# Kernel tuning notes

Hardware: AMD Instinct MI355X
Metric: run time of the kernel (lower is better)

## Reference

```python
import jax, jax.numpy as jnp
import numpy as np

D_MODEL = 1024
NUM_HEADS = 16
DEPTH = D_MODEL // NUM_HEADS


def setup_inputs() -> dict:
    key = jax.random.key(0)
    ks = jax.random.split(key, 11)
    B, S, D = 2, 2048, D_MODEL
    s = 1.0 / np.sqrt(D)
    inp = {
        'x': jax.random.normal(ks[0], (B, S, D), jnp.float32),
        'pH': jax.random.normal(ks[1], (B, 1, 1), jnp.float32),
        'Wq': jax.random.normal(ks[2], (D, D), jnp.float32) * s,
        'bq': jnp.zeros((D,), jnp.float32),
        'Wk': jax.random.normal(ks[3], (D, D), jnp.float32) * s,
        'bk': jnp.zeros((D,), jnp.float32),
        'Wv': jax.random.normal(ks[4], (D, D), jnp.float32) * s,
        'bv': jnp.zeros((D,), jnp.float32),
        'Wo': jax.random.normal(ks[5], (D, D), jnp.float32) * s,
        'bo': jnp.zeros((D,), jnp.float32),
    }
    return inp


def reference(x, pH, Wq, bq, Wk, bk, Wv, bv, Wo, bo):
    B, S, D = x.shape
    H, dh = NUM_HEADS, DEPTH
    # QKV projections -> [B, H, S, dh]
    def proj(W, b):
        return (x @ W + b).reshape(B, S, H, dh).transpose(0, 2, 1, 3)
    q = proj(Wq, bq)
    k = proj(Wk, bk)
    v = proj(Wv, bv)
    # scores [B, H, S, S] with additive per-sample pH bias broadcast over heads/positions
    scores = jnp.einsum('bhqd,bhkd->bhqk', q, k) / jnp.sqrt(jnp.asarray(dh, x.dtype))
    scores = scores + pH[:, :, :, None]  # [B,1,1,1] broadcasts to [B,H,S,S]
    attn = jax.nn.softmax(scores, axis=-1)
    out = jnp.einsum('bhqk,bhkd->bhqd', attn, v)  # [B,H,S,dh]
    out = out.transpose(0, 2, 1, 3).reshape(B, S, D)
    return out @ Wo + bo  # dropout p=0.0 -> identity
```

## Files before the change

### kernel.cpp

```cpp
#include <hip/hip_runtime.h>
#include <hip/hip_bf16.h>
#include <math.h>

#define BATCH 2
#define SEQ   2048
#define DMODEL 1024
#define NHEADS 16
#define DHEAD 64
#define MROWS (BATCH*SEQ)

typedef __attribute__((ext_vector_type(8))) short bf16x8;
typedef __attribute__((ext_vector_type(4))) short bf16x4;
typedef __attribute__((ext_vector_type(4))) float f32x4;

__device__ __forceinline__ short f2bf(float f) {
    union { float f; unsigned u; } c; c.f = f;
    unsigned r = (c.u + 0x7fffu + ((c.u >> 16) & 1u)) >> 16;
    return (short)r;
}
__device__ __forceinline__ float bf2f(short h) {
    union { unsigned u; float f; } c; c.u = ((unsigned)(unsigned short)h) << 16;
    return c.f;
}

__device__ __forceinline__ void async_ld16(const void* g, void* l) {
    __builtin_amdgcn_global_load_lds(
        (const __attribute__((address_space(1))) unsigned*)g,
        (__attribute__((address_space(3))) unsigned*)l, 16, 0, 0);
}

__global__ __launch_bounds__(256) void prep(
    const float* __restrict__ x, short* __restrict__ xhi,
    const float* __restrict__ W0, const float* __restrict__ W1,
    const float* __restrict__ W2, const float* __restrict__ W3,
    short* __restrict__ oqkv, short* __restrict__ oo)
{
    __shared__ float T[64][65];
    const int tid = threadIdx.x;
    if (blockIdx.x < 2048) {
        const int i = blockIdx.x * 256 + tid;
        const float4* p = (const float4*)x + (size_t)i * 2;
        float4 a = p[0], b = p[1];
        float v[8] = {a.x, a.y, a.z, a.w, b.x, b.y, b.z, b.w};
        bf16x8 H;
        #pragma unroll
        for (int j = 0; j < 8; ++j) H[j] = f2bf(v[j]);
        *((bf16x8*)xhi + i) = H;
        return;
    }
    const int bi = blockIdx.x - 2048;
    const int z = bi >> 8;
    const int t = bi & 255;
    const float* W = (z == 0) ? W0 : (z == 1) ? W1 : (z == 2) ? W2 : W3;
    short* out = (z < 3) ? (oqkv + (size_t)z * 1024 * 1024) : oo;
    const int n0 = (t & 15) * 64, k0 = (t >> 4) * 64;
    #pragma unroll
    for (int i = 0; i < 16; ++i) {
        const int idx = tid + i * 256;
        const int r = idx >> 6, c = idx & 63;
        T[r][c] = W[(size_t)(k0 + r) * DMODEL + n0 + c];
    }
    __syncthreads();
    #pragma unroll
    for (int i = 0; i < 4; ++i) {
        const int idx = tid + i * 256;
        const int r = idx >> 4, g = idx & 15;
        bf16x4 H;
        #pragma unroll
        for (int j = 0; j < 4; ++j)
            H[j] = f2bf(T[g * 4 + j][r]);
        *(bf16x4*)(out + (size_t)(n0 + r) * DMODEL + k0 + g * 4) = H;
    }
}

#define GBK 64

__global__ __launch_bounds__(256) void mfma_gemm(
    const short* __restrict__ Ahi, const short* __restrict__ Bthi,
    const float* __restrict__ b0, const float* __restrict__ b1, const float* __restrict__ b2,
    short* __restrict__ oqh, short* __restrict__ okh, short* __restrict__ ovh,
    float* __restrict__ outf, int mode, float qscale)
{
    __shared__ short Ah[128 * GBK], Bh[128 * GBK];

    const int tid  = threadIdx.x;
    const int lane = tid & 63;
    const int w    = tid >> 6;
    const int quad = lane >> 4;
    const int l15  = lane & 15;
    const int wr   = w >> 1, wc = w & 1;
    const int m0   = blockIdx.y * 128;
    const int n0   = blockIdx.x * 128;
    const int K    = DMODEL;

    f32x4 acc[4][4] = {};

    int srow[4], spos[4];
    #pragma unroll
    for (int j = 0; j < 4; ++j) {
        const int c = w * 256 + j * 64 + lane;
        srow[j] = c >> 3;
        spos[j] = (c & 7) ^ (srow[j] & 7);
    }

    for (int k0 = 0; k0 < K; k0 += GBK) {
        __syncthreads();
        #pragma unroll
        for (int j = 0; j < 4; ++j) {
            const int cB = (w * 256 + j * 64) * 8;
            async_ld16(Ahi + (size_t)(m0 + srow[j]) * K + k0 + spos[j] * 8, Ah + cB);
            async_ld16(Bthi + (size_t)(n0 + srow[j]) * K + k0 + spos[j] * 8, Bh + cB);
        }
        __syncthreads();

        #pragma unroll
        for (int s = 0; s < 2; ++s) {
            bf16x8 afh[4], bfh[4];
            #pragma unroll
            for (int mi = 0; mi < 4; ++mi) {
                const int row = wr * 64 + mi * 16 + l15;
                const int pos = (s * 4 + quad) ^ (row & 7);
                afh[mi] = *(const bf16x8*)(Ah + row * GBK + pos * 8);
            }
            #pragma unroll
            for (int ni = 0; ni < 4; ++ni) {
                const int row = wc * 64 + ni * 16 + l15;
                const int pos = (s * 4 + quad) ^ (row & 7);
                bfh[ni] = *(const bf16x8*)(Bh + row * GBK + pos * 8);
            }
            #pragma unroll
            for (int mi = 0; mi < 4; ++mi)
                #pragma unroll
                for (int ni = 0; ni < 4; ++ni)
                    acc[mi][ni] = __builtin_amdgcn_mfma_f32_16x16x32_bf16(
                        afh[mi], bfh[ni], acc[mi][ni], 0, 0, 0);
        }
    }

    const int nbase = n0 + wc * 64;
    if (mode == 1) {
        #pragma unroll
        for (int mi = 0; mi < 4; ++mi)
            #pragma unroll
            for (int ni = 0; ni < 4; ++ni)
                #pragma unroll
                for (int r = 0; r < 4; ++r) {
                    const int m = m0 + wr * 64 + mi * 16 + quad * 4 + r;
                    const int nn = nbase + ni * 16 + l15;
                    outf[(size_t)m * DMODEL + nn] = acc[mi][ni][r] + b0[nn];
                }
    } else {
        __syncthreads();
        short* scr = (w < 2) ? (Ah + w * 4096) : (Bh + (w - 2) * 4096);
        const int which = nbase >> 10;
        const int hh = (nbase & 1023) >> 6;
        const int mb = m0 + wr * 64;
        const int b = mb >> 11, sbase = mb & (SEQ - 1);

        if (which < 2) {
            const float* bias = which ? b1 : b0;
            short* dstp = which ? okh : oqh;
            const float scl = which ? 1.0f : qscale;
            #pragma unroll
            for (int mi = 0; mi < 4; ++mi)
                #pragma unroll
                for (int ni = 0; ni < 4; ++ni)
                    #pragma unroll
                    for (int r = 0; r < 4; ++r) {
                        const int sloc = mi * 16 + quad * 4 + r;
                        const int dloc = ni * 16 + l15;
                        const int nn = (nbase + ni * 16 + l15) & 1023;
                        scr[sloc * 64 + (((dloc >> 3) ^ (sloc & 7)) * 8) + (dloc & 7)] =
                            f2bf((acc[mi][ni][r] + bias[nn]) * scl);
                    }
            #pragma unroll
            for (int i = 0; i < 8; ++i) {
                const int sloc = i * 8 + (lane >> 3);
                const int cph = (lane & 7) ^ (sloc & 7);
                bf16x8 row = *(const bf16x8*)(scr + sloc * 64 + cph * 8);
                const int dloc = (lane & 7) * 8;
                *(bf16x8*)(dstp + ((size_t)(b * NHEADS + hh) * SEQ + sbase + sloc) * DHEAD + dloc) = row;
            }
        } else {
            #pragma unroll
            for (int mi = 0; mi < 4; ++mi)
                #pragma unroll
                for (int ni = 0; ni < 4; ++ni)
                    #pragma unroll
                    for (int r = 0; r < 4; ++r) {
                        const int sloc = mi * 16 + quad * 4 + r;
                        const int dloc = ni * 16 + l15;
                        const int nn = (nbase + ni * 16 + l15) & 1023;
                        scr[dloc * 64 + (((sloc >> 3) ^ (dloc & 7)) * 8) + (sloc & 7)] =
                            f2bf(acc[mi][ni][r] + b2[nn]);
                    }
            #pragma unroll
            for (int i = 0; i < 8; ++i) {
                const int dloc = i * 8 + (lane >> 3);
                const int cph = (lane & 7) ^ (dloc & 7);
                bf16x8 row = *(const bf16x8*)(scr + dloc * 64 + cph * 8);
                const int sg = sbase + (lane & 7) * 8;
                *(bf16x8*)(ovh + ((size_t)(b * NHEADS + hh) * DHEAD + dloc) * SEQ + sg) = row;
            }
        }
    }
}

__global__ __launch_bounds__(256) void attn_mfma(
    const short* __restrict__ Qh_g, const short* __restrict__ Kh_g,
    const short* __restrict__ Vth_g,
    short* __restrict__ op0, short* __restrict__ op1,
    float* __restrict__ l0g, float* __restrict__ l1g)
{
    __shared__ short Ksh[4096];
    __shared__ short Vsh[4096];
    __shared__ short Ph[4][2][1024];

    const int tid  = threadIdx.x;
    const int lane = tid & 63;
    const int w    = tid >> 6;
    const int quad = lane >> 4;
    const int l15  = lane & 15;

    const int bh    = blockIdx.x & 31;
    const int sk    = (blockIdx.x >> 5) & 1;
    const int qtile = blockIdx.x >> 6;
    const int q0    = qtile * 128 + w * 32;
    const size_t kvb = (size_t)bh * SEQ * DHEAD;

    bf16x8 ones;
    #pragma unroll
    for (int j = 0; j < 8; ++j) ones[j] = (short)0x3f80;

    bf16x8 qA[2], qB[2];
    {
        const size_t qrA = kvb + (size_t)(q0 + l15) * DHEAD;
        const size_t qrB = kvb + (size_t)(q0 + 16 + l15) * DHEAD;
        qA[0] = *(const bf16x8*)(Qh_g + qrA + quad * 8);
        qA[1] = *(const bf16x8*)(Qh_g + qrA + 32 + quad * 8);
        qB[0] = *(const bf16x8*)(Qh_g + qrB + quad * 8);
        qB[1] = *(const bf16x8*)(Qh_g + qrB + 32 + quad * 8);
    }

    const bool isv = (w >= 2);
    short* dst = isv ? Vsh : Ksh;
    int srow[4], spos[4];
    #pragma unroll
    for (int j = 0; j < 4; ++j) {
        const int c = (w & 1) * 256 + j * 64 + lane;
        srow[j] = c >> 3;
        spos[j] = (c & 7) ^ (srow[j] & 7);
    }

    f32x4 oA[4] = {}, oB[4] = {};
    f32x4 lAv = {}, lBv = {};

    const int kb0 = sk * (SEQ / 2), kb1 = kb0 + SEQ / 2;
    for (int kb = kb0; kb < kb1; kb += 64) {
        __syncthreads();
        {
            const short* src = isv ? (Vth_g + kvb + kb) : (Kh_g + kvb + (size_t)kb * DHEAD);
            #pragma unroll
            for (int j = 0; j < 4; ++j) {
                const short* g = src + (isv ? ((size_t)srow[j] * SEQ + spos[j] * 8)
                                            : ((size_t)srow[j] * DHEAD + spos[j] * 8));
                async_ld16(g, dst + ((w & 1) * 256 + j * 64) * 8);
            }
        }
        __syncthreads();

        #pragma unroll
        for (int mf = 0; mf < 4; ++mf) {
            const int row = mf * 16 + l15;
            const int sw = row & 7;
            bf16x8 kh0 = *(const bf16x8*)(Ksh + row * 64 + ((quad ^ sw) * 8));
            bf16x8 kh1 = *(const bf16x8*)(Ksh + row * 64 + (((4 + quad) ^ sw) * 8));
            f32x4 cA = {}, cB = {};
            cA = __builtin_amdgcn_mfma_f32_16x16x32_bf16(kh0, qA[0], cA, 0, 0, 0);
            cA = __builtin_amdgcn_mfma_f32_16x16x32_bf16(kh1, qA[1], cA, 0, 0, 0);
            cB = __builtin_amdgcn_mfma_f32_16x16x32_bf16(kh0, qB[0], cB, 0, 0, 0);
            cB = __builtin_amdgcn_mfma_f32_16x16x32_bf16(kh1, qB[1], cB, 0, 0, 0);

            unsigned uA[4], uB[4];
            #pragma unroll
            for (int r = 0; r < 4; ++r) {
                union { float f; unsigned u; } p;
                p.f = __builtin_amdgcn_exp2f(cA[r]);
                uA[r] = p.u;
                p.f = __builtin_amdgcn_exp2f(cB[r]);
                uB[r] = p.u;
            }
            uint2 pkA, pkB;
            pkA.x = __builtin_amdgcn_perm(uA[1], uA[0], 0x07060302u);
            pkA.y = __builtin_amdgcn_perm(uA[3], uA[2], 0x07060302u);
            pkB.x = __builtin_amdgcn_perm(uB[1], uB[0], 0x07060302u);
            pkB.y = __builtin_amdgcn_perm(uB[3], uB[2], 0x07060302u);
            const int pc = (mf * 2 + (quad >> 1)) ^ (l15 & 7);
            const int paddr = l15 * 64 + pc * 8 + (quad & 1) * 4;
            *(uint2*)(&Ph[w][0][paddr]) = pkA;
            *(uint2*)(&Ph[w][1][paddr]) = pkB;
        }

        const int psw = l15 & 7;
        bf16x8 pA0 = *(const bf16x8*)(&Ph[w][0][l15 * 64 + ((quad ^ psw) * 8)]);
        bf16x8 pA1 = *(const bf16x8*)(&Ph[w][0][l15 * 64 + (((4 + quad) ^ psw) * 8)]);
        bf16x8 pB0 = *(const bf16x8*)(&Ph[w][1][l15 * 64 + ((quad ^ psw) * 8)]);
        bf16x8 pB1 = *(const bf16x8*)(&Ph[w][1][l15 * 64 + (((4 + quad) ^ psw) * 8)]);

        lAv = __builtin_amdgcn_mfma_f32_16x16x32_bf16(pA0, ones, lAv, 0, 0, 0);
        lAv = __builtin_amdgcn_mfma_f32_16x16x32_bf16(pA1, ones, lAv, 0, 0, 0);
        lBv = __builtin_amdgcn_mfma_f32_16x16x32_bf16(pB0, ones, lBv, 0, 0, 0);
        lBv = __builtin_amdgcn_mfma_f32_16x16x32_bf16(pB1, ones, lBv, 0, 0, 0);

        #pragma unroll
        for (int nf = 0; nf < 4; ++nf) {
            const int row = nf * 16 + l15;
            const int sw = row & 7;
            bf16x8 vh0 = *(const bf16x8*)(Vsh + row * 64 + ((quad ^ sw) * 8));
            bf16x8 vh1 = *(const bf16x8*)(Vsh + row * 64 + (((4 + quad) ^ sw) * 8));
            f32x4 cA = oA[nf], cB = oB[nf];
            cA = __builtin_amdgcn_mfma_f32_16x16x32_bf16(pA0, vh0, cA, 0, 0, 0);
            cA = __builtin_amdgcn_mfma_f32_16x16x32_bf16(pA1, vh1, cA, 0, 0, 0);
            cB = __builtin_amdgcn_mfma_f32_16x16x32_bf16(pB0, vh0, cB, 0, 0, 0);
            cB = __builtin_amdgcn_mfma_f32_16x16x32_bf16(pB1, vh1, cB, 0, 0, 0);
            oA[nf] = cA; oB[nf] = cB;
        }
    }

    short* op = sk ? op1 : op0;
    float* lg = sk ? l1g : l0g;
    const int b = bh >> 4, hh = bh & 15;
    #pragma unroll
    for (int r = 0; r < 4; ++r) {
        const int qa = q0 + quad * 4 + r;
        if (l15 == 0) {
            lg[bh * SEQ + qa] = lAv[r];
            lg[bh * SEQ + qa + 16] = lBv[r];
        }
    }
    #pragma unroll
    for (int nf = 0; nf < 4; ++nf) {
        #pragma unroll
        for (int r = 0; r < 4; ++r) {
            const int qa = q0 + quad * 4 + r;
            const int d = nf * 16 + l15;
            op[(size_t)(b * SEQ + qa) * DMODEL + hh * DHEAD + d] = f2bf(oA[nf][r]);
            op[(size_t)(b * SEQ + qa + 16) * DMODEL + hh * DHEAD + d] = f2bf(oB[nf][r]);
        }
    }
}

__global__ __launch_bounds__(256) void combine_o(
    const short* __restrict__ op0, const short* __restrict__ op1,
    const float* __restrict__ l0g, const float* __restrict__ l1g,
    short* __restrict__ aoh)
{
    const int i = blockIdx.x * 256 + threadIdx.x;
    const size_t e = (size_t)i * 8;
    const int qg = (int)(e >> 10);
    const int col = (int)(e & 1023);
    const int b = qg >> 11;
    const int q = qg & (SEQ - 1);
    const int bh = b * NHEADS + (col >> 6);
    const float inv = 1.0f / (l0g[bh * SEQ + q] + l1g[bh * SEQ + q]);

    bf16x8 a = *((const bf16x8*)op0 + i);
    bf16x8 c = *((const bf16x8*)op1 + i);
    bf16x8 H;
    #pragma unroll
    for (int j = 0; j < 8; ++j)
        H[j] = f2bf((bf2f(a[j]) + bf2f(c[j])) * inv);
    *((bf16x8*)aoh + i) = H;
}

extern "C" void kernel_launch(void* const* d_in, const int* in_sizes, int n_in,
                              void* d_out, int out_size, void* d_ws, size_t ws_size,
                              hipStream_t stream) {
    const float* x  = (const float*)d_in[0];
    const float* Wq = (const float*)d_in[2];
    const float* bq = (const float*)d_in[3];
    const float* Wk = (const float*)d_in[4];
    const float* bk = (const float*)d_in[5];
    const float* Wv = (const float*)d_in[6];
    const float* bv = (const float*)d_in[7];
    const float* Wo = (const float*)d_in[8];
    const float* bo = (const float*)d_in[9];
    float* out = (float*)d_out;

    char* ws = (char*)d_ws;
    const size_t MB = 1024 * 1024;
    short* qh  = (short*)(ws + 0 * MB);
    short* kh  = (short*)(ws + 16 * MB);
    short* vth = (short*)(ws + 32 * MB);
    short* aoh = (short*)(ws + 48 * MB);
    short* op0 = (short*)(ws + 56 * MB);
    short* xhi = (short*)(ws + 64 * MB);
    short* op1 = (short*)(ws + 72 * MB);
    short* wqkv_hi = (short*)(ws + 80 * MB);
    float* l0g = (float*)(ws + 88 * MB);
    float* l1g = (float*)(ws + 89 * MB);
    short* wto_hi  = (short*)(ws + 92 * MB);

    dim3 blk(256);

    hipLaunchKernelGGL(prep, dim3(2048 + 1024), blk, 0, stream,
                       x, xhi, Wq, Wk, Wv, Wo, wqkv_hi, wto_hi);

    const float qscale = 0.125f * 1.44269504088896f;
    hipLaunchKernelGGL(mfma_gemm, dim3(3072 / 128, MROWS / 128), blk, 0, stream,
                       xhi, wqkv_hi, bq, bk, bv,
                       qh, kh, vth, (float*)nullptr, 0, qscale);

    hipLaunchKernelGGL(attn_mfma, dim3(BATCH * NHEADS * (SEQ / 128) * 2), blk, 0, stream,
                       qh, kh, vth, op0, op1, l0g, l1g);

    hipLaunchKernelGGL(combine_o, dim3(MROWS * DMODEL / 8 / 256), blk, 0, stream,
                       op0, op1, l0g, l1g, aoh);

    hipLaunchKernelGGL(mfma_gemm, dim3(1024 / 128, MROWS / 128), blk, 0, stream,
                       aoh, wto_hi, bo, bo, bo,
                       (short*)nullptr, (short*)nullptr, (short*)nullptr,
                       out, 1, 1.0f);
}
```

Measured before the change: 205.9 us.

## Split attention keys four ways and give output projection smaller tiles

The attention kernel now splits the key range into four partial passes instead of two. The combine kernel sums four partial outputs and four row-sum buffers, all stored at strided offsets in the workspace. The output projection moves to a dedicated GEMM kernel with 64x128 tiles, which doubles its block count and simplifies the QKV GEMM by dropping its mode flag. The aim is more blocks in flight per CU, at the cost of extra partial-output memory traffic and reduction work in the combine step.

```diff
diff --git a/kernel.cpp b/kernel.cpp
--- a/kernel.cpp
+++ b/kernel.cpp
@@ -79,7 +79,7 @@
     const short* __restrict__ Ahi, const short* __restrict__ Bthi,
     const float* __restrict__ b0, const float* __restrict__ b1, const float* __restrict__ b2,
     short* __restrict__ oqh, short* __restrict__ okh, short* __restrict__ ovh,
-    float* __restrict__ outf, int mode, float qscale)
+    float qscale)
 {
     __shared__ short Ah[128 * GBK], Bh[128 * GBK];
 
@@ -138,93 +138,150 @@
     }
 
     const int nbase = n0 + wc * 64;
-    if (mode == 1) {
+    __syncthreads();
+    short* scr = (w < 2) ? (Ah + w * 4096) : (Bh + (w - 2) * 4096);
+    const int which = nbase >> 10;
+    const int hh = (nbase & 1023) >> 6;
+    const int mb = m0 + wr * 64;
+    const int b = mb >> 11, sbase = mb & (SEQ - 1);
+
+    if (which < 2) {
+        const float* bias = which ? b1 : b0;
+        short* dstp = which ? okh : oqh;
+        const float scl = which ? 1.0f : qscale;
         #pragma unroll
         for (int mi = 0; mi < 4; ++mi)
             #pragma unroll
             for (int ni = 0; ni < 4; ++ni)
                 #pragma unroll
                 for (int r = 0; r < 4; ++r) {
-                    const int m = m0 + wr * 64 + mi * 16 + quad * 4 + r;
-                    const int nn = nbase + ni * 16 + l15;
-                    outf[(size_t)m * DMODEL + nn] = acc[mi][ni][r] + b0[nn];
+                    const int sloc = mi * 16 + quad * 4 + r;
+                    const int dloc = ni * 16 + l15;
+                    const int nn = (nbase + ni * 16 + l15) & 1023;
+                    scr[sloc * 64 + (((dloc >> 3) ^ (sloc & 7)) * 8) + (dloc & 7)] =
+                        f2bf((acc[mi][ni][r] + bias[nn]) * scl);
                 }
+        #pragma unroll
+        for (int i = 0; i < 8; ++i) {
+            const int sloc = i * 8 + (lane >> 3);
+            const int cph = (lane & 7) ^ (sloc & 7);
+            bf16x8 row = *(const bf16x8*)(scr + sloc * 64 + cph * 8);
+            const int dloc = (lane & 7) * 8;
+            *(bf16x8*)(dstp + ((size_t)(b * NHEADS + hh) * SEQ + sbase + sloc) * DHEAD + dloc) = row;
+        }
     } else {
-        __syncthreads();
-        short* scr = (w < 2) ? (Ah + w * 4096) : (Bh + (w - 2) * 4096);
-        const int which = nbase >> 10;
-        const int hh = (nbase & 1023) >> 6;
-        const int mb = m0 + wr * 64;
-        const int b = mb >> 11, sbase = mb & (SEQ - 1);
-
-        if (which < 2) {
-            const float* bias = which ? b1 : b0;
-            short* dstp = which ? okh : oqh;
-            const float scl = which ? 1.0f : qscale;
-            #pragma unroll
-            for (int mi = 0; mi < 4; ++mi)
+        #pragma unroll
+        for (int mi = 0; mi < 4; ++mi)
+            #pragma unroll
+            for (int ni = 0; ni < 4; ++ni)
                 #pragma unroll
-                for (int ni = 0; ni < 4; ++ni)
-                    #pragma unroll
-                    for (int r = 0; r < 4; ++r) {
-                        const int sloc = mi * 16 + quad * 4 + r;
-                        const int dloc = ni * 16 + l15;
-                        const int nn = (nbase + ni * 16 + l15) & 1023;
-                        scr[sloc * 64 + (((dloc >> 3) ^ (sloc & 7)) * 8) + (dloc & 7)] =
-                            f2bf((acc[mi][ni][r] + bias[nn]) * scl);
-                    }
-            #pragma unroll
-            for (int i = 0; i < 8; ++i) {
-                const int sloc = i * 8 + (lane >> 3);
-                const int cph = (lane & 7) ^ (sloc & 7);
-                bf16x8 row = *(const bf16x8*)(scr + sloc * 64 + cph * 8);
-                const int dloc = (lane & 7) * 8;
-                *(bf16x8*)(dstp + ((size_t)(b * NHEADS + hh) * SEQ + sbase + sloc) * DHEAD + dloc) = row;
-            }
-        } else {
-            #pragma unroll
-            for (int mi = 0; mi < 4; ++mi)
-                #pragma unroll
-                for (int ni = 0; ni < 4; ++ni)
-                    #pragma unroll
-                    for (int r = 0; r < 4; ++r) {
-                        const int sloc = mi * 16 + quad * 4 + r;
-                        const int dloc = ni * 16 + l15;
-                        const int nn = (nbase + ni * 16 + l15) & 1023;
-                        scr[dloc * 64 + (((sloc >> 3) ^ (dloc & 7)) * 8) + (sloc & 7)] =
-                            f2bf(acc[mi][ni][r] + b2[nn]);
-                    }
-            #pragma unroll
-            for (int i = 0; i < 8; ++i) {
-                const int dloc = i * 8 + (lane >> 3);
-                const int cph = (lane & 7) ^ (dloc & 7);
-                bf16x8 row = *(const bf16x8*)(scr + dloc * 64 + cph * 8);
-                const int sg = sbase + (lane & 7) * 8;
-                *(bf16x8*)(ovh + ((size_t)(b * NHEADS + hh) * DHEAD + dloc) * SEQ + sg) = row;
-            }
-        }
-    }
-}
-
-__global__ __launch_bounds__(256) void attn_mfma(
-    const short* __restrict__ Qh_g, const short* __restrict__ Kh_g,
-    const short* __restrict__ Vth_g,
-    short* __restrict__ op0, short* __restrict__ op1,
-    float* __restrict__ l0g, float* __restrict__ l1g)
+                for (int r = 0; r < 4; ++r) {
+                    const int sloc = mi * 16 + quad * 4 + r;
+                    const int dloc = ni * 16 + l15;
+                    const int nn = (nbase + ni * 16 + l15) & 1023;
+                    scr[dloc * 64 + (((sloc >> 3) ^ (dloc & 7)) * 8) + (sloc & 7)] =
+                        f2bf(acc[mi][ni][r] + b2[nn]);
+                }
+        #pragma unroll
+        for (int i = 0; i < 8; ++i) {
+            const int dloc = i * 8 + (lane >> 3);
+            const int cph = (lane & 7) ^ (dloc & 7);
+            bf16x8 row = *(const bf16x8*)(scr + dloc * 64 + cph * 8);
+            const int sg = sbase + (lane & 7) * 8;
+            *(bf16x8*)(ovh + ((size_t)(b * NHEADS + hh) * DHEAD + dloc) * SEQ + sg) = row;
+        }
+    }
+}
+
+__global__ __launch_bounds__(256) void ogemm(
+    const short* __restrict__ Ahi, const short* __restrict__ Bthi,
+    const float* __restrict__ b0, float* __restrict__ outf)
 {
-    __shared__ short Ksh[4096];
-    __shared__ short Vsh[4096];
-    __shared__ short Ph[4][2][1024];
+    __shared__ short Ah[64 * 64], Bh[128 * 64];
 
     const int tid  = threadIdx.x;
     const int lane = tid & 63;
     const int w    = tid >> 6;
     const int quad = lane >> 4;
     const int l15  = lane & 15;
+    const int wr   = w >> 1, wc = w & 1;
+    const int m0   = blockIdx.y * 64;
+    const int n0   = blockIdx.x * 128;
+    const int K    = DMODEL;
+
+    f32x4 acc[2][4] = {};
+
+    for (int k0 = 0; k0 < K; k0 += 64) {
+        __syncthreads();
+        #pragma unroll
+        for (int j = 0; j < 6; ++j) {
+            const int base = w * 384 + j * 64;
+            const int c = base + lane;
+            if (base < 512) {
+                const int row = c >> 3, pos = (c & 7) ^ (row & 7);
+                async_ld16(Ahi + (size_t)(m0 + row) * K + k0 + pos * 8, Ah + base * 8);
+            } else {
+                const int cb = c - 512;
+                const int row = cb >> 3, pos = (cb & 7) ^ (row & 7);
+                async_ld16(Bthi + (size_t)(n0 + row) * K + k0 + pos * 8, Bh + (base - 512) * 8);
+            }
+        }
+        __syncthreads();
+
+        #pragma unroll
+        for (int s = 0; s < 2; ++s) {
+            bf16x8 afh[2], bfh[4];
+            #pragma unroll
+            for (int mi = 0; mi < 2; ++mi) {
+                const int row = wr * 32 + mi * 16 + l15;
+                const int pos = (s * 4 + quad) ^ (row & 7);
+                afh[mi] = *(const bf16x8*)(Ah + row * 64 + pos * 8);
+            }
+            #pragma unroll
+            for (int ni = 0; ni < 4; ++ni) {
+                const int row = wc * 64 + ni * 16 + l15;
+                const int pos = (s * 4 + quad) ^ (row & 7);
+                bfh[ni] = *(const bf16x8*)(Bh + row * 64 + pos * 8);
+            }
+            #pragma unroll
+            for (int mi = 0; mi < 2; ++mi)
+                #pragma unroll
+                for (int ni = 0; ni < 4; ++ni)
+                    acc[mi][ni] = __builtin_amdgcn_mfma_f32_16x16x32_bf16(
+                        afh[mi], bfh[ni], acc[mi][ni], 0, 0, 0);
+        }
+    }
+
+    #pragma unroll
+    for (int mi = 0; mi < 2; ++mi)
+        #pragma unroll
+        for (int ni = 0; ni < 4; ++ni)
+            #pragma unroll
+            for (int r = 0; r < 4; ++r) {
+                const int m = m0 + wr * 32 + mi * 16 + quad * 4 + r;
+                const int nn = n0 + wc * 64 + ni * 16 + l15;
+                outf[(size_t)m * DMODEL + nn] = acc[mi][ni][r] + b0[nn];
+            }
+}
+
+__global__ __launch_bounds__(256) void attn_mfma(
+    const short* __restrict__ Qh_g, const short* __restrict__ Kh_g,
+    const short* __restrict__ Vth_g,
+    short* __restrict__ op0, float* __restrict__ l0g)
+{
+    __shared__ short Ksh[4096];
+    __shared__ short Vsh[4096];
+    __shared__ short Ph[4][2][1024];
+
+    const int tid  = threadIdx.x;
+    const int lane = tid & 63;
+    const int w    = tid >> 6;
+    const int quad = lane >> 4;
+    const int l15  = lane & 15;
 
     const int bh    = blockIdx.x & 31;
-    const int sk    = (blockIdx.x >> 5) & 1;
-    const int qtile = blockIdx.x >> 6;
+    const int sk    = (blockIdx.x >> 5) & 3;
+    const int qtile = blockIdx.x >> 7;
     const int q0    = qtile * 128 + w * 32;
     const size_t kvb = (size_t)bh * SEQ * DHEAD;
 
@@ -255,7 +312,7 @@
     f32x4 oA[4] = {}, oB[4] = {};
     f32x4 lAv = {}, lBv = {};
 
-    const int kb0 = sk * (SEQ / 2), kb1 = kb0 + SEQ / 2;
+    const int kb0 = sk * (SEQ / 4), kb1 = kb0 + SEQ / 4;
     for (int kb = kb0; kb < kb1; kb += 64) {
         __syncthreads();
         {
@@ -327,8 +384,8 @@
         }
     }
 
-    short* op = sk ? op1 : op0;
-    float* lg = sk ? l1g : l0g;
+    short* op = op0 + (size_t)sk * 4194304;
+    float* lg = l0g + sk * 65536;
     const int b = bh >> 4, hh = bh & 15;
     #pragma unroll
     for (int r = 0; r < 4; ++r) {
@@ -351,8 +408,7 @@
 }
 
 __global__ __launch_bounds__(256) void combine_o(
-    const short* __restrict__ op0, const short* __restrict__ op1,
-    const float* __restrict__ l0g, const float* __restrict__ l1g,
+    const short* __restrict__ op0, const float* __restrict__ l0g,
     short* __restrict__ aoh)
 {
     const int i = blockIdx.x * 256 + threadIdx.x;
@@ -361,15 +417,18 @@
     const int col = (int)(e & 1023);
     const int b = qg >> 11;
     const int q = qg & (SEQ - 1);
-    const int bh = b * NHEADS + (col >> 6);
-    const float inv = 1.0f / (l0g[bh * SEQ + q] + l1g[bh * SEQ + q]);
-
-    bf16x8 a = *((const bf16x8*)op0 + i);
-    bf16x8 c = *((const bf16x8*)op1 + i);
+    const int bhq = (b * NHEADS + (col >> 6)) * SEQ + q;
+    const float inv = 1.0f / (l0g[bhq] + l0g[bhq + 65536] +
+                              l0g[bhq + 2 * 65536] + l0g[bhq + 3 * 65536]);
+
+    bf16x8 a0 = *((const bf16x8*)op0 + i);
+    bf16x8 a1 = *((const bf16x8*)(op0 + 4194304) + i);
+    bf16x8 a2 = *((const bf16x8*)(op0 + 2 * 4194304) + i);
+    bf16x8 a3 = *((const bf16x8*)(op0 + 3 * 4194304) + i);
     bf16x8 H;
     #pragma unroll
     for (int j = 0; j < 8; ++j)
-        H[j] = f2bf((bf2f(a[j]) + bf2f(c[j])) * inv);
+        H[j] = f2bf((bf2f(a0[j]) + bf2f(a1[j]) + bf2f(a2[j]) + bf2f(a3[j])) * inv);
     *((bf16x8*)aoh + i) = H;
 }
 
@@ -395,10 +454,8 @@
     short* aoh = (short*)(ws + 48 * MB);
     short* op0 = (short*)(ws + 56 * MB);
     short* xhi = (short*)(ws + 64 * MB);
-    short* op1 = (short*)(ws + 72 * MB);
     short* wqkv_hi = (short*)(ws + 80 * MB);
     float* l0g = (float*)(ws + 88 * MB);
-    float* l1g = (float*)(ws + 89 * MB);
     short* wto_hi  = (short*)(ws + 92 * MB);
 
     dim3 blk(256);
@@ -408,17 +465,14 @@
 
     const float qscale = 0.125f * 1.44269504088896f;
     hipLaunchKernelGGL(mfma_gemm, dim3(3072 / 128, MROWS / 128), blk, 0, stream,
-                       xhi, wqkv_hi, bq, bk, bv,
-                       qh, kh, vth, (float*)nullptr, 0, qscale);
-
-    hipLaunchKernelGGL(attn_mfma, dim3(BATCH * NHEADS * (SEQ / 128) * 2), blk, 0, stream,
-                       qh, kh, vth, op0, op1, l0g, l1g);
+                       xhi, wqkv_hi, bq, bk, bv, qh, kh, vth, qscale);
+
+    hipLaunchKernelGGL(attn_mfma, dim3(BATCH * NHEADS * (SEQ / 128) * 4), blk, 0, stream,
+                       qh, kh, vth, op0, l0g);
 
     hipLaunchKernelGGL(combine_o, dim3(MROWS * DMODEL / 8 / 256), blk, 0, stream,
-                       op0, op1, l0g, l1g, aoh);
-
-    hipLaunchKernelGGL(mfma_gemm, dim3(1024 / 128, MROWS / 128), blk, 0, stream,
-                       aoh, wto_hi, bo, bo, bo,
-                       (short*)nullptr, (short*)nullptr, (short*)nullptr,
-                       out, 1, 1.0f);
-}
+                       op0, l0g, aoh);
+
+    hipLaunchKernelGGL(ogemm, dim3(1024 / 128, MROWS / 64), blk, 0, stream,
+                       aoh, wto_hi, bo, out);
+}
```

New measurement: 205.4 us. No clear change (-0.2%).
